# Optimization experiments

Measured on AMD Instinct MI355X. Metric: run time of the kernel, lower is better.

## Reference

```python
import jax, jax.numpy as jnp
import numpy as np

N = 100000      # nodes
E = 1600000     # edges (avg degree 16)
F_IN = 128      # node feature dim
F_OUT = 128     # GCN output dim


def setup_inputs() -> dict:
    key = jax.random.key(0)
    ks = jax.random.split(key, 11)
    s = 0.05  # weight scale to keep activations sane
    return {
        "x": jax.random.normal(ks[0], (N, F_IN), jnp.float32),
        "edge_index": jax.random.randint(ks[1], (2, E), 0, N, jnp.int32),
        "W": jax.random.normal(ks[2], (F_IN, F_OUT), jnp.float32) * s,
        "p": jax.random.normal(ks[3], (F_IN,), jnp.float32),
        "w_ih": jax.random.normal(ks[4], (3 * F_OUT, F_IN), jnp.float32) * s,
        "w_hh": jax.random.normal(ks[5], (3 * F_OUT, F_OUT), jnp.float32) * s,
        "b_ih": jax.random.normal(ks[6], (3 * F_OUT,), jnp.float32) * s,
        "b_hh": jax.random.normal(ks[7], (3 * F_OUT,), jnp.float32) * s,
        "conv_bias": jax.random.normal(ks[8], (F_OUT,), jnp.float32) * s,
        "lin_w": jax.random.normal(ks[9], (1, F_OUT), jnp.float32) * s,
        "lin_b": jax.random.normal(ks[10], (1,), jnp.float32) * s,
    }


def reference(x, edge_index, W, p, w_ih, w_hh, b_ih, b_hh, conv_bias, lin_w, lin_b):
    n_nodes = x.shape[0]
    k, H = W.shape  # k = F_IN rows, H = F_OUT hidden size

    # --- TopK summarize: pick k nodes, gate by tanh(score) -> X_tilde [k, F_IN]
    scores = x @ p / jnp.linalg.norm(p)
    top_vals, top_idx = jax.lax.top_k(scores, k)
    x_tilde = x[top_idx] * jnp.tanh(top_vals)[:, None]

    # --- one GRU step evolving W (hidden state = rows of W)
    gi = x_tilde @ w_ih.T + b_ih   # [k, 3H]
    gh = W @ w_hh.T + b_hh         # [k, 3H]
    r = jax.nn.sigmoid(gi[:, :H] + gh[:, :H])
    z = jax.nn.sigmoid(gi[:, H:2 * H] + gh[:, H:2 * H])
    n = jnp.tanh(gi[:, 2 * H:] + r * gh[:, 2 * H:])
    W_new = (1.0 - z) * n + z * W  # [F_IN, F_OUT]

    # --- GCN conv with fixed W: sym-normalized adjacency with self loops
    row, col = edge_index[0], edge_index[1]
    deg = jax.ops.segment_sum(jnp.ones_like(row, dtype=x.dtype), col,
                              num_segments=n_nodes) + 1.0  # +1 for self loop
    dinv = jax.lax.rsqrt(deg)
    xw = x @ W_new                                   # [N, F_OUT]
    coef = dinv[row] * dinv[col]                     # [E]
    agg = jax.ops.segment_sum(xw[row] * coef[:, None], col, num_segments=n_nodes)
    agg = agg + xw * (dinv * dinv)[:, None] + conv_bias  # self-loop term + bias

    # --- head: ReLU + Linear(F_OUT, 1)
    h = jax.nn.relu(agg)
    return h @ lin_w.T + lin_b  # [N, 1]
```

## Files before the change

kernel.cpp:

```cpp
#include <hip/hip_runtime.h>
#include <math.h>

#define N_NODES 100000
#define N_EDGES 1600000
#define F 128

#define BSH 9
#define NBUCK 196
#define BCAP 10240
#define PB_EDGES 4096

typedef unsigned int u32;
typedef unsigned short u16;
typedef __attribute__((ext_vector_type(8))) short short8;
typedef __attribute__((ext_vector_type(4))) float floatx4;


__device__ __forceinline__ u32 key_of(float s) {
    u32 u = __float_as_uint(s);
    return (u & 0x80000000u) ? ~u : (u | 0x80000000u);
}

__device__ __forceinline__ float wave_reduce(float v) {
    #pragma unroll
    for (int off = 32; off > 0; off >>= 1) v += __shfl_down(v, off, 64);
    return v;
}

__device__ __forceinline__ u16 f2bf(float f) {
    u32 u = __float_as_uint(f);
    u += 0x7fffu + ((u >> 16) & 1u);
    return (u16)(u >> 16);
}

__device__ __forceinline__ float bflo(u32 b) { return __uint_as_float(b << 16); }
__device__ __forceinline__ float bfhi(u32 b) { return __uint_as_float(b & 0xffff0000u); }


__global__ void k_scores(const float* __restrict__ x, const float* __restrict__ p,
                         float* __restrict__ scores, u32* __restrict__ hist16) {
    int node = blockIdx.x * 4 + (threadIdx.x >> 6);
    int lane = threadIdx.x & 63;
    if (node >= N_NODES) return;
    float2 xv = *(const float2*)&x[(size_t)node * F + lane * 2];
    float2 pv = *(const float2*)&p[lane * 2];
    float d = xv.x * pv.x + xv.y * pv.y;
    d = wave_reduce(d);
    if (lane == 0) {
        scores[node] = d;
        atomicAdd(&hist16[key_of(d) >> 16], 1u);
    }
}


__global__ __launch_bounds__(1024) void k_scan16(const u32* __restrict__ hist16,
                                                 u32* __restrict__ state) {
    __shared__ u32 a[1024];
    int t = threadIdx.x;
    const uint4* h4 = (const uint4*)hist16;
    u32 local = 0;
    #pragma unroll
    for (int i = 0; i < 16; i++) {
        uint4 v = h4[t * 16 + i];
        local += v.x + v.y + v.z + v.w;
    }
    a[t] = local;
    __syncthreads();
    for (int off = 1; off < 1024; off <<= 1) {
        u32 add = (t + off < 1024) ? a[t + off] : 0u;
        __syncthreads();
        a[t] += add;
        __syncthreads();
    }
    u32 S_above = (t == 1023) ? 0u : a[t + 1];
    if (S_above < 128u && a[t] >= 128u) {
        u32 cum = S_above;
        for (int v = t * 64 + 63; v >= t * 64; v--) {
            cum += hist16[v];
            if (cum >= 128u) { state[0] = (u32)v; break; }
        }
    }
}

__global__ void k_collect16(const float* __restrict__ scores, u32* __restrict__ state,
                            u32* __restrict__ cand) {
    u32 T = state[0] << 16;
    int i = blockIdx.x * blockDim.x + threadIdx.x;
    if (i < N_NODES) {
        if (key_of(scores[i]) >= T) {
            u32 pos = atomicAdd(&state[2], 1u);
            if (pos < 2048u) cand[pos] = (u32)i;
        }
    }
}

__global__ void k_assemble16(const float* __restrict__ scores, const float* __restrict__ p,
                             const u32* __restrict__ state, const u32* __restrict__ cand,
                             u32* __restrict__ top_idx, float* __restrict__ gate) {
    __shared__ u32 ci[2048];
    __shared__ float csc[2048];
    __shared__ float s_inv;
    int t = threadIdx.x;
    if (t < 64) {
        float2 pv = *(const float2*)&p[t * 2];
        float d = pv.x * pv.x + pv.y * pv.y;
        d = wave_reduce(d);
        if (t == 0) s_inv = rsqrtf(d);
    }
    u32 nc = state[2]; if (nc > 2048u) nc = 2048u;
    for (u32 i = t; i < nc; i += 256) { u32 ix = cand[i]; ci[i] = ix; csc[i] = scores[ix]; }
    __syncthreads();
    for (u32 i = t; i < nc; i += 256) {
        u32 myk = key_of(csc[i]);
        u32 myi = ci[i];
        int rank = 0;
        for (u32 j = 0; j < nc; j++) {
            u32 ok = key_of(csc[j]);
            rank += (int)((ok > myk) || (ok == myk && ci[j] < myi));
        }
        if (rank < 128) {
            top_idx[rank] = myi;
            gate[rank] = tanhf(csc[i] * s_inv);
        }
    }
}


__global__ __launch_bounds__(256) void k_ggemm(const float* __restrict__ x,
                                               const float* __restrict__ W,
                                               const float* __restrict__ w_ih,
                                               const float* __restrict__ w_hh,
                                               const u32* __restrict__ top_idx,
                                               const float* __restrict__ gate,
                                               float* __restrict__ G) {
    __shared__ float As[32][128];
    __shared__ float Bs[64][131];
    int t = threadIdx.x;
    int k0 = blockIdx.x * 32;
    int by = blockIdx.y;
    int j0 = by * 64;
    bool is_gi = (by < 6);
    #pragma unroll
    for (int i = 0; i < 4; i++) {
        int l = t + i * 256;
        int row = l >> 5, c4 = l & 31;
        float4 v;
        if (is_gi) {
            u32 idx = top_idx[k0 + row];
            float gt = gate[k0 + row];
            v = *(const float4*)&x[(size_t)idx * F + c4 * 4];
            v.x *= gt; v.y *= gt; v.z *= gt; v.w *= gt;
        } else {
            v = *(const float4*)&W[(k0 + row) * F + c4 * 4];
        }
        *(float4*)&As[row][c4 * 4] = v;
    }
    const float* mat = is_gi ? w_ih : w_hh;
    int jbase = is_gi ? j0 : (j0 - 384);
    #pragma unroll
    for (int i = 0; i < 8; i++) {
        int l = t + i * 256;
        int row = l >> 5, c4 = l & 31;
        float4 v = *(const float4*)&mat[(jbase + row) * F + c4 * 4];
        Bs[row][c4 * 4 + 0] = v.x; Bs[row][c4 * 4 + 1] = v.y;
        Bs[row][c4 * 4 + 2] = v.z; Bs[row][c4 * 4 + 3] = v.w;
    }
    __syncthreads();
    int ty = t >> 5, tx = t & 31;
    float acc[4][2] = {};
    #pragma unroll 4
    for (int f = 0; f < 128; f++) {
        float b0 = Bs[tx * 2][f], b1 = Bs[tx * 2 + 1][f];
        #pragma unroll
        for (int i = 0; i < 4; i++) {
            float a = As[ty * 4 + i][f];
            acc[i][0] += a * b0;
            acc[i][1] += a * b1;
        }
    }
    #pragma unroll
    for (int i = 0; i < 4; i++) {
        int k = k0 + ty * 4 + i;
        G[(size_t)k * 768 + j0 + tx * 2 + 0] = acc[i][0];
        G[(size_t)k * 768 + j0 + tx * 2 + 1] = acc[i][1];
    }
}


__global__ void k_gate(const float* __restrict__ G, const float* __restrict__ W,
                       const float* __restrict__ b_ih, const float* __restrict__ b_hh,
                       float* __restrict__ Wnew, u16* __restrict__ Bfrag) {
    int idx = blockIdx.x * blockDim.x + threadIdx.x;
    int k = idx >> 7, h = idx & 127;
    const float* gk = &G[(size_t)k * 768];
    float gir = gk[h]       + b_ih[h];
    float giz = gk[128 + h] + b_ih[128 + h];
    float gin = gk[256 + h] + b_ih[256 + h];
    float ghr = gk[384 + h] + b_hh[h];
    float ghz = gk[512 + h] + b_hh[128 + h];
    float ghn = gk[640 + h] + b_hh[256 + h];
    float wv  = W[k * F + h];
    float rg = 1.0f / (1.0f + expf(-(gir + ghr)));
    float z  = 1.0f / (1.0f + expf(-(giz + ghz)));
    float n  = tanhf(gin + rg * ghn);
    float val = (1.0f - z) * n + z * wv;
    Wnew[k * F + h] = val;
    int nb = h >> 4, kc = k >> 5, q = (k >> 3) & 3, m = h & 15, jj = k & 7;
    Bfrag[(((nb * 4 + kc) * 64) + q * 16 + m) * 8 + jj] = f2bf(val);
}


__global__ void k_part(const int* __restrict__ ei, u32* __restrict__ gcur,
                       u32* __restrict__ pairs) {
    __shared__ u32 lh[NBUCK];
    __shared__ u32 lbase[NBUCK];
    int t = threadIdx.x;
    int e0 = blockIdx.x * PB_EDGES;
    int e1 = e0 + PB_EDGES; if (e1 > N_EDGES) e1 = N_EDGES;
    for (int i = t; i < NBUCK; i += 256) lh[i] = 0u;
    __syncthreads();
    for (int e = e0 + t; e < e1; e += 256)
        atomicAdd(&lh[((u32)ei[N_EDGES + e]) >> BSH], 1u);
    __syncthreads();
    for (int b = t; b < NBUCK; b += 256) {
        u32 c = lh[b];
        lbase[b] = c ? atomicAdd(&gcur[b], c) : 0u;
        lh[b] = 0u;
    }
    __syncthreads();
    for (int e = e0 + t; e < e1; e += 256) {
        u32 d = (u32)ei[N_EDGES + e];
        u32 b = d >> BSH;
        u32 pos = lbase[b] + atomicAdd(&lh[b], 1u);
        pairs[(size_t)b * BCAP + pos] = ((d & 511u) << 17) | (u32)ei[e];
    }
}

__global__ __launch_bounds__(256) void k_csr(const u32* __restrict__ pairs,
                                             const u32* __restrict__ gcur,
                                             u32* __restrict__ offs,
                                             float* __restrict__ dinv,
                                             u32* __restrict__ ebuf) {
    __shared__ u32 h[512];
    __shared__ u32 sc[512];
    __shared__ u32 ps[256];
    int b = blockIdx.x, t = threadIdx.x;
    u32 pv = (t < NBUCK) ? gcur[t] : 0u;
    ps[t] = pv;
    __syncthreads();
    for (int off = 1; off < 256; off <<= 1) {
        u32 add = (t >= off) ? ps[t - off] : 0u;
        __syncthreads();
        ps[t] += add;
        __syncthreads();
    }
    u32 base = ps[b] - gcur[b];
    u32 cnt  = gcur[b];
    const u32* seg = pairs + (size_t)b * BCAP;
    u32 lo = (u32)b << BSH;
    for (int i = t; i < 512; i += 256) h[i] = 0u;
    __syncthreads();
    for (u32 i = t; i < cnt; i += 256)
        atomicAdd(&h[seg[i] >> 17], 1u);
    __syncthreads();
    for (int i = t; i < 512; i += 256) sc[i] = h[i];
    __syncthreads();
    for (int off = 1; off < 512; off <<= 1) {
        int i0 = t, i1 = t + 256;
        u32 v0 = (i0 >= off) ? sc[i0 - off] : 0u;
        u32 v1 = (i1 >= off) ? sc[i1 - off] : 0u;
        __syncthreads();
        sc[i0] += v0; sc[i1] += v1;
        __syncthreads();
    }
    int nn = N_NODES - (int)lo; if (nn > 512) nn = 512;
    for (int i = t; i < nn; i += 256) {
        u32 c = h[i];
        offs[lo + i] = base + (sc[i] - c);
        dinv[lo + i] = rsqrtf((float)c + 1.0f);
    }
    for (int i = t; i < 512; i += 256) sc[i] -= h[i];
    __syncthreads();
    for (u32 i = t; i < cnt; i += 256) {
        u32 pr = seg[i];
        u32 pos = base + atomicAdd(&sc[pr >> 17], 1u);
        ebuf[pos] = pr & 0x1ffffu;
    }
    if (b == 0 && t == 0) offs[N_NODES] = N_EDGES;
}


__global__ __launch_bounds__(256) void k_gemm(const float* __restrict__ x,
                                              const u16* __restrict__ Bfrag,
                                              u16* __restrict__ xwh) {
    __shared__ __align__(16) u16 As[8192];
    __shared__ __align__(16) u16 Bs[16384];
    int t = threadIdx.x;
    int r0 = blockIdx.x * 64;
    #pragma unroll
    for (int i = 0; i < 8; i++) {
        int l = t + i * 256;
        int row = l >> 5, c4 = l & 31;
        int f0 = c4 * 4;
        float4 v = {0.f, 0.f, 0.f, 0.f};
        if (r0 + row < N_NODES) v = *(const float4*)&x[(size_t)(r0 + row) * F + f0];
        int widx = (((row >> 4) * 4 + (f0 >> 5)) * 64 + ((f0 >> 3) & 3) * 16 + (row & 15)) * 8
                   + (f0 & 7);
        ushort4 s4;
        s4.x = f2bf(v.x); s4.y = f2bf(v.y); s4.z = f2bf(v.z); s4.w = f2bf(v.w);
        *(ushort4*)&As[widx] = s4;
    }
    #pragma unroll
    for (int i = 0; i < 8; i++) {
        int idx = t + i * 256;
        ((uint4*)Bs)[idx] = ((const uint4*)Bfrag)[idx];
    }
    __syncthreads();

    int wv = t >> 6, lane = t & 63;
    floatx4 acc[8] = {};
    #pragma unroll
    for (int kc = 0; kc < 4; kc++) {
        short8 a = *(const short8*)&As[((wv * 4 + kc) * 64 + lane) * 8];
        #pragma unroll
        for (int nb = 0; nb < 8; nb++) {
            short8 b = *(const short8*)&Bs[((nb * 4 + kc) * 64 + lane) * 8];
            acc[nb] = __builtin_amdgcn_mfma_f32_16x16x32_bf16(a, b, acc[nb], 0, 0, 0);
        }
    }
    int q = lane >> 4, m = lane & 15;
    #pragma unroll
    for (int nb = 0; nb < 8; nb++) {
        #pragma unroll
        for (int reg = 0; reg < 4; reg++) {
            int grow = r0 + wv * 16 + q * 4 + reg;
            if (grow < N_NODES)
                xwh[(size_t)grow * F + nb * 16 + m] = f2bf(acc[nb][reg]);
        }
    }
}


#define EDGE_GROUP(J) {                                                      \
    u32 r = ebuf[(J) + q];                                                   \
    float wv = dinv[r];                                                      \
    uint4 bb = *(const uint4*)&xw32[(size_t)r * 64 + sub * 4];               \
    a0 += wv * bflo(bb.x); a1 += wv * bfhi(bb.x);                            \
    a2 += wv * bflo(bb.y); a3 += wv * bfhi(bb.y);                            \
    a4 += wv * bflo(bb.z); a5 += wv * bfhi(bb.z);                            \
    a6 += wv * bflo(bb.w); a7 += wv * bfhi(bb.w); }

__global__ void k_gather(const u32* __restrict__ xw32, const u32* __restrict__ offs,
                         const u32* __restrict__ ebuf, const float* __restrict__ dinv,
                         const float* __restrict__ conv_bias, const float* __restrict__ lin_w,
                         const float* __restrict__ lin_b, float* __restrict__ out) {
    int c = blockIdx.x * 4 + (threadIdx.x >> 6);
    if (c >= N_NODES) return;
    int lane = threadIdx.x & 63;
    int q = lane >> 4, sub = lane & 15;
    u32 jbeg = offs[c], jend = offs[c + 1];
    float a0 = 0.f, a1 = 0.f, a2 = 0.f, a3 = 0.f;
    float a4 = 0.f, a5 = 0.f, a6 = 0.f, a7 = 0.f;
    u32 j = jbeg;
    for (; j + 16 <= jend; j += 16) {
        EDGE_GROUP(j) EDGE_GROUP(j + 4) EDGE_GROUP(j + 8) EDGE_GROUP(j + 12)
    }
    for (; j + 4 <= jend; j += 4) EDGE_GROUP(j)
    u32 rem = jend - j;
    if (rem) {
        u32 idx = ((u32)q < rem) ? (j + q) : (jend - 1);
        u32 r = ebuf[idx];
        float wv = ((u32)q < rem) ? dinv[r] : 0.f;
        uint4 bb = *(const uint4*)&xw32[(size_t)r * 64 + sub * 4];
        a0 += wv * bflo(bb.x); a1 += wv * bfhi(bb.x);
        a2 += wv * bflo(bb.y); a3 += wv * bfhi(bb.y);
        a4 += wv * bflo(bb.z); a5 += wv * bfhi(bb.z);
        a6 += wv * bflo(bb.w); a7 += wv * bfhi(bb.w);
    }
    a0 += __shfl_xor(a0, 16, 64); a0 += __shfl_xor(a0, 32, 64);
    a1 += __shfl_xor(a1, 16, 64); a1 += __shfl_xor(a1, 32, 64);
    a2 += __shfl_xor(a2, 16, 64); a2 += __shfl_xor(a2, 32, 64);
    a3 += __shfl_xor(a3, 16, 64); a3 += __shfl_xor(a3, 32, 64);
    a4 += __shfl_xor(a4, 16, 64); a4 += __shfl_xor(a4, 32, 64);
    a5 += __shfl_xor(a5, 16, 64); a5 += __shfl_xor(a5, 32, 64);
    a6 += __shfl_xor(a6, 16, 64); a6 += __shfl_xor(a6, 32, 64);
    a7 += __shfl_xor(a7, 16, 64); a7 += __shfl_xor(a7, 32, 64);
    float dc = dinv[c], d2 = dc * dc;
    uint4 sb = *(const uint4*)&xw32[(size_t)c * 64 + sub * 4];
    float4 cb0 = *(const float4*)&conv_bias[sub * 8];
    float4 cb1 = *(const float4*)&conv_bias[sub * 8 + 4];
    float4 lw0 = *(const float4*)&lin_w[sub * 8];
    float4 lw1 = *(const float4*)&lin_w[sub * 8 + 4];
    float h0 = fmaxf(dc * a0 + d2 * bflo(sb.x) + cb0.x, 0.f);
    float h1 = fmaxf(dc * a1 + d2 * bfhi(sb.x) + cb0.y, 0.f);
    float h2 = fmaxf(dc * a2 + d2 * bflo(sb.y) + cb0.z, 0.f);
    float h3 = fmaxf(dc * a3 + d2 * bfhi(sb.y) + cb0.w, 0.f);
    float h4 = fmaxf(dc * a4 + d2 * bflo(sb.z) + cb1.x, 0.f);
    float h5 = fmaxf(dc * a5 + d2 * bfhi(sb.z) + cb1.y, 0.f);
    float h6 = fmaxf(dc * a6 + d2 * bflo(sb.w) + cb1.z, 0.f);
    float h7 = fmaxf(dc * a7 + d2 * bfhi(sb.w) + cb1.w, 0.f);
    float part = (h0 * lw0.x + h1 * lw0.y + h2 * lw0.z + h3 * lw0.w)
               + (h4 * lw1.x + h5 * lw1.y + h6 * lw1.z + h7 * lw1.w);
    part = (q == 0) ? part : 0.f;
    part = wave_reduce(part);
    if (lane == 0) out[c] = part + lin_b[0];
}


extern "C" void kernel_launch(void* const* d_in, const int* in_sizes, int n_in,
                              void* d_out, int out_size, void* d_ws, size_t ws_size,
                              hipStream_t stream) {
    const float* x         = (const float*)d_in[0];
    const int*   ei        = (const int*)  d_in[1];
    const float* W         = (const float*)d_in[2];
    const float* p         = (const float*)d_in[3];
    const float* w_ih      = (const float*)d_in[4];
    const float* w_hh      = (const float*)d_in[5];
    const float* b_ih      = (const float*)d_in[6];
    const float* b_hh      = (const float*)d_in[7];
    const float* conv_bias = (const float*)d_in[8];
    const float* lin_w     = (const float*)d_in[9];
    const float* lin_b     = (const float*)d_in[10];
    float* out = (float*)d_out;

    u32*   w  = (u32*)d_ws;
    float* wf = (float*)d_ws;

    const size_t SCORES_W = 0;
    const size_t DINV_W   = 100096;
    const size_t OFFS_W   = 200192;
    const size_t HIST16_W = 300288;
    const size_t STATE_W  = 365824;
    const size_t GCUR_W   = 365832;
    const size_t CAND_W   = 366080;
    const size_t TOPI_W   = 368128;
    const size_t GATE_W   = 368256;
    const size_t WNEW_W   = 368384;
    const size_t BFRAG_W  = 384768;
    const size_t PAIRS_W  = 392960;
    const size_t EBUF_W   = 2400000;
    const size_t XW_W     = 4000000;

    float* scores  = wf + SCORES_W;
    float* dinv    = wf + DINV_W;
    u32*   offs    = w  + OFFS_W;
    u32*   hist16  = w  + HIST16_W;
    u32*   state   = w  + STATE_W;
    u32*   gcur    = w  + GCUR_W;
    u32*   cand    = w  + CAND_W;
    u32*   top_idx = w  + TOPI_W;
    float* gate    = wf + GATE_W;
    float* Wnew    = wf + WNEW_W;
    u16*   Bfrag   = (u16*)(w + BFRAG_W);
    u32*   pairs   = w  + PAIRS_W;
    float* G       = wf + PAIRS_W;
    u32*   ebuf    = w  + EBUF_W;
    u16*   xwh     = (u16*)(w + XW_W);
    u32*   xw32    = w + XW_W;

    hipMemsetAsync(hist16, 0, (65536 + 8 + NBUCK) * sizeof(u32), stream);

    k_scores<<<25000, 256, 0, stream>>>(x, p, scores, hist16);
    k_scan16<<<1, 1024, 0, stream>>>(hist16, state);
    k_collect16<<<392, 256, 0, stream>>>(scores, state, cand);
    k_assemble16<<<1, 256, 0, stream>>>(scores, p, state, cand, top_idx, gate);
    k_ggemm<<<dim3(4, 12), 256, 0, stream>>>(x, W, w_ih, w_hh, top_idx, gate, G);
    k_gate<<<64, 256, 0, stream>>>(G, W, b_ih, b_hh, Wnew, Bfrag);

    k_gemm<<<1563, 256, 0, stream>>>(x, Bfrag, xwh);

    k_part<<<(N_EDGES + PB_EDGES - 1) / PB_EDGES, 256, 0, stream>>>(ei, gcur, pairs);
    k_csr<<<NBUCK, 256, 0, stream>>>(pairs, gcur, offs, dinv, ebuf);

    k_gather<<<25000, 256, 0, stream>>>(xw32, offs, ebuf, dinv, conv_bias, lin_w,
                                        lin_b, out);
}
```

Baseline: 330.6 us.

## Prescale GEMM output by dinv and stage stores through LDS for coalescing

Measured after the change: 326.3 us. No clear change (-1.3%).

```diff
diff --git a/kernel.cpp b/kernel.cpp
--- a/kernel.cpp
+++ b/kernel.cpp
@@ -292,9 +292,9 @@
 
 __global__ __launch_bounds__(256) void k_gemm(const float* __restrict__ x,
                                               const u16* __restrict__ Bfrag,
-                                              u16* __restrict__ xwh) {
-    __shared__ __align__(16) u16 As[8192];
-    __shared__ __align__(16) u16 Bs[16384];
+                                              const float* __restrict__ dinv,
+                                              u16* __restrict__ yw) {
+    __shared__ __align__(16) u16 As[8448];
     int t = threadIdx.x;
     int r0 = blockIdx.x * 64;
     #pragma unroll
@@ -310,32 +310,45 @@
         s4.x = f2bf(v.x); s4.y = f2bf(v.y); s4.z = f2bf(v.z); s4.w = f2bf(v.w);
         *(ushort4*)&As[widx] = s4;
     }
-    #pragma unroll
-    for (int i = 0; i < 8; i++) {
-        int idx = t + i * 256;
-        ((uint4*)Bs)[idx] = ((const uint4*)Bfrag)[idx];
-    }
     __syncthreads();
 
     int wv = t >> 6, lane = t & 63;
+    int q = lane >> 4, m = lane & 15;
     floatx4 acc[8] = {};
     #pragma unroll
     for (int kc = 0; kc < 4; kc++) {
         short8 a = *(const short8*)&As[((wv * 4 + kc) * 64 + lane) * 8];
         #pragma unroll
         for (int nb = 0; nb < 8; nb++) {
-            short8 b = *(const short8*)&Bs[((nb * 4 + kc) * 64 + lane) * 8];
-            acc[nb] = __builtin_amdgcn_mfma_f32_16x16x32_bf16(a, b, acc[nb], 0, 0, 0);
-        }
-    }
-    int q = lane >> 4, m = lane & 15;
+            short8 bfr = *(const short8*)&Bfrag[((nb * 4 + kc) * 64 + lane) * 8];
+            acc[nb] = __builtin_amdgcn_mfma_f32_16x16x32_bf16(a, bfr, acc[nb], 0, 0, 0);
+        }
+    }
+    __syncthreads();
+
+    float d[4];
+    #pragma unroll
+    for (int reg = 0; reg < 4; reg++) {
+        int gr = r0 + wv * 16 + q * 4 + reg;
+        d[reg] = (gr < N_NODES) ? dinv[gr] : 0.f;
+    }
     #pragma unroll
     for (int nb = 0; nb < 8; nb++) {
         #pragma unroll
         for (int reg = 0; reg < 4; reg++) {
-            int grow = r0 + wv * 16 + q * 4 + reg;
-            if (grow < N_NODES)
-                xwh[(size_t)grow * F + nb * 16 + m] = f2bf(acc[nb][reg]);
+            int row = wv * 16 + q * 4 + reg;
+            As[row * 132 + nb * 16 + m] = f2bf(acc[nb][reg] * d[reg]);
+        }
+    }
+    __syncthreads();
+    {
+        int row = t >> 2, segi = t & 3;
+        int gr = r0 + row;
+        if (gr < N_NODES) {
+            const uint2* src = (const uint2*)&As[row * 132 + segi * 32];
+            uint2* dst = (uint2*)&yw[(size_t)gr * F + segi * 32];
+            #pragma unroll
+            for (int i = 0; i < 8; i++) dst[i] = src[i];
         }
     }
 }
@@ -343,14 +356,13 @@
 
 #define EDGE_GROUP(J) {                                                      \
     u32 r = ebuf[(J) + q];                                                   \
-    float wv = dinv[r];                                                      \
-    uint4 bb = *(const uint4*)&xw32[(size_t)r * 64 + sub * 4];               \
-    a0 += wv * bflo(bb.x); a1 += wv * bfhi(bb.x);                            \
-    a2 += wv * bflo(bb.y); a3 += wv * bfhi(bb.y);                            \
-    a4 += wv * bflo(bb.z); a5 += wv * bfhi(bb.z);                            \
-    a6 += wv * bflo(bb.w); a7 += wv * bfhi(bb.w); }
-
-__global__ void k_gather(const u32* __restrict__ xw32, const u32* __restrict__ offs,
+    uint4 bb = *(const uint4*)&yw32[(size_t)r * 64 + sub * 4];               \
+    a0 += bflo(bb.x); a1 += bfhi(bb.x);                                      \
+    a2 += bflo(bb.y); a3 += bfhi(bb.y);                                      \
+    a4 += bflo(bb.z); a5 += bfhi(bb.z);                                      \
+    a6 += bflo(bb.w); a7 += bfhi(bb.w); }
+
+__global__ void k_gather(const u32* __restrict__ yw32, const u32* __restrict__ offs,
                          const u32* __restrict__ ebuf, const float* __restrict__ dinv,
                          const float* __restrict__ conv_bias, const float* __restrict__ lin_w,
                          const float* __restrict__ lin_b, float* __restrict__ out) {
@@ -370,12 +382,12 @@
     if (rem) {
         u32 idx = ((u32)q < rem) ? (j + q) : (jend - 1);
         u32 r = ebuf[idx];
-        float wv = ((u32)q < rem) ? dinv[r] : 0.f;
-        uint4 bb = *(const uint4*)&xw32[(size_t)r * 64 + sub * 4];
-        a0 += wv * bflo(bb.x); a1 += wv * bfhi(bb.x);
-        a2 += wv * bflo(bb.y); a3 += wv * bfhi(bb.y);
-        a4 += wv * bflo(bb.z); a5 += wv * bfhi(bb.z);
-        a6 += wv * bflo(bb.w); a7 += wv * bfhi(bb.w);
+        float mk = ((u32)q < rem) ? 1.f : 0.f;
+        uint4 bb = *(const uint4*)&yw32[(size_t)r * 64 + sub * 4];
+        a0 += mk * bflo(bb.x); a1 += mk * bfhi(bb.x);
+        a2 += mk * bflo(bb.y); a3 += mk * bfhi(bb.y);
+        a4 += mk * bflo(bb.z); a5 += mk * bfhi(bb.z);
+        a6 += mk * bflo(bb.w); a7 += mk * bfhi(bb.w);
     }
     a0 += __shfl_xor(a0, 16, 64); a0 += __shfl_xor(a0, 32, 64);
     a1 += __shfl_xor(a1, 16, 64); a1 += __shfl_xor(a1, 32, 64);
@@ -385,20 +397,20 @@
     a5 += __shfl_xor(a5, 16, 64); a5 += __shfl_xor(a5, 32, 64);
     a6 += __shfl_xor(a6, 16, 64); a6 += __shfl_xor(a6, 32, 64);
     a7 += __shfl_xor(a7, 16, 64); a7 += __shfl_xor(a7, 32, 64);
-    float dc = dinv[c], d2 = dc * dc;
-    uint4 sb = *(const uint4*)&xw32[(size_t)c * 64 + sub * 4];
+    float dc = dinv[c];
+    uint4 sb = *(const uint4*)&yw32[(size_t)c * 64 + sub * 4];
     float4 cb0 = *(const float4*)&conv_bias[sub * 8];
     float4 cb1 = *(const float4*)&conv_bias[sub * 8 + 4];
     float4 lw0 = *(const float4*)&lin_w[sub * 8];
     float4 lw1 = *(const float4*)&lin_w[sub * 8 + 4];
-    float h0 = fmaxf(dc * a0 + d2 * bflo(sb.x) + cb0.x, 0.f);
-    float h1 = fmaxf(dc * a1 + d2 * bfhi(sb.x) + cb0.y, 0.f);
-    float h2 = fmaxf(dc * a2 + d2 * bflo(sb.y) + cb0.z, 0.f);
-    float h3 = fmaxf(dc * a3 + d2 * bfhi(sb.y) + cb0.w, 0.f);
-    float h4 = fmaxf(dc * a4 + d2 * bflo(sb.z) + cb1.x, 0.f);
-    float h5 = fmaxf(dc * a5 + d2 * bfhi(sb.z) + cb1.y, 0.f);
-    float h6 = fmaxf(dc * a6 + d2 * bflo(sb.w) + cb1.z, 0.f);
-    float h7 = fmaxf(dc * a7 + d2 * bfhi(sb.w) + cb1.w, 0.f);
+    float h0 = fmaxf(dc * (a0 + bflo(sb.x)) + cb0.x, 0.f);
+    float h1 = fmaxf(dc * (a1 + bfhi(sb.x)) + cb0.y, 0.f);
+    float h2 = fmaxf(dc * (a2 + bflo(sb.y)) + cb0.z, 0.f);
+    float h3 = fmaxf(dc * (a3 + bfhi(sb.y)) + cb0.w, 0.f);
+    float h4 = fmaxf(dc * (a4 + bflo(sb.z)) + cb1.x, 0.f);
+    float h5 = fmaxf(dc * (a5 + bfhi(sb.z)) + cb1.y, 0.f);
+    float h6 = fmaxf(dc * (a6 + bflo(sb.w)) + cb1.z, 0.f);
+    float h7 = fmaxf(dc * (a7 + bfhi(sb.w)) + cb1.w, 0.f);
     float part = (h0 * lw0.x + h1 * lw0.y + h2 * lw0.z + h3 * lw0.w)
                + (h4 * lw1.x + h5 * lw1.y + h6 * lw1.z + h7 * lw1.w);
     part = (q == 0) ? part : 0.f;
@@ -439,7 +451,7 @@
     const size_t BFRAG_W  = 384768;
     const size_t PAIRS_W  = 392960;
     const size_t EBUF_W   = 2400000;
-    const size_t XW_W     = 4000000;
+    const size_t YW_W     = 4000000;
 
     float* scores  = wf + SCORES_W;
     float* dinv    = wf + DINV_W;
@@ -455,8 +467,8 @@
     u32*   pairs   = w  + PAIRS_W;
     float* G       = wf + PAIRS_W;
     u32*   ebuf    = w  + EBUF_W;
-    u16*   xwh     = (u16*)(w + XW_W);
-    u32*   xw32    = w + XW_W;
+    u16*   yw      = (u16*)(w + YW_W);
+    u32*   yw32    = w + YW_W;
 
     hipMemsetAsync(hist16, 0, (65536 + 8 + NBUCK) * sizeof(u32), stream);
 
@@ -464,14 +476,15 @@
     k_scan16<<<1, 1024, 0, stream>>>(hist16, state);
     k_collect16<<<392, 256, 0, stream>>>(scores, state, cand);
     k_assemble16<<<1, 256, 0, stream>>>(scores, p, state, cand, top_idx, gate);
+
     k_ggemm<<<dim3(4, 12), 256, 0, stream>>>(x, W, w_ih, w_hh, top_idx, gate, G);
     k_gate<<<64, 256, 0, stream>>>(G, W, b_ih, b_hh, Wnew, Bfrag);
 
-    k_gemm<<<1563, 256, 0, stream>>>(x, Bfrag, xwh);
-
     k_part<<<(N_EDGES + PB_EDGES - 1) / PB_EDGES, 256, 0, stream>>>(ei, gcur, pairs);
     k_csr<<<NBUCK, 256, 0, stream>>>(pairs, gcur, offs, dinv, ebuf);
 
-    k_gather<<<25000, 256, 0, stream>>>(xw32, offs, ebuf, dinv, conv_bias, lin_w,
+    k_gemm<<<1563, 256, 0, stream>>>(x, Bfrag, dinv, yw);
+
+    k_gather<<<25000, 256, 0, stream>>>(yw32, offs, ebuf, dinv, conv_bias, lin_w,
                                         lin_b, out);
 }
```
